# Performance work log

Measured on AMD Instinct MI355X. Metric: run time of the kernel, lower is better.

Reference implementation:

```python
import jax, jax.numpy as jnp
import numpy as np

B, S, E, D, H = 64, 4096, 512, 512, 512
NEG = -1.0e9

def setup_inputs() -> dict:
    key = jax.random.key(0)
    k1, k2, k3, k4, k5, k6 = jax.random.split(key, 6)
    return {
        "enc": jax.random.normal(k1, (B, S, E), dtype=jnp.float32),
        "dec": jax.random.normal(k2, (B, D), dtype=jnp.float32),
        "inp_mask": jax.random.randint(k3, (B, S), 0, 2, dtype=jnp.int32),
        "W_enc": jax.random.normal(k4, (E, H), dtype=jnp.float32),
        "W_dec": jax.random.normal(k5, (D, H), dtype=jnp.float32),
        "W_out": jax.random.normal(k6, (H, 1), dtype=jnp.float32),
    }

def reference(enc, dec, inp_mask, W_enc, W_dec, W_out):
    # Bahdanau additive attention
    encoded = enc @ W_enc                     # [B,S,H]
    decoded = dec @ W_dec                     # [B,H]
    result = jnp.tanh(encoded + decoded[:, None, :])   # [B,S,H]
    logits = jnp.squeeze(result @ W_out, -1)  # [B,S]
    logits = jnp.where(inp_mask == 0, NEG, logits)
    probs = jax.nn.softmax(logits, axis=1)    # [B,S]
    attn = jnp.einsum('bse,bs->be', enc, probs)  # [B,E]
    return (attn, probs)
```

## Files before the change

### kernel.cpp

```cpp
#include <hip/hip_runtime.h>
#include <hip/hip_bf16.h>
#include <cstdint>
#include <cstddef>

#define B_ 64
#define S_ 4096
#define E_ 512
#define H_ 512
#define NEGV (-1.0e9f)

typedef short s8v __attribute__((ext_vector_type(8)));
typedef float f4v __attribute__((ext_vector_type(4)));

__device__ __forceinline__ unsigned short f2bf(float x) {
    unsigned u = __builtin_bit_cast(unsigned, x);
    u = u + 0x7FFFu + ((u >> 16) & 1u);
    return (unsigned short)(u >> 16);
}
__device__ __forceinline__ float bf2f(unsigned short h) {
    unsigned u = ((unsigned)h) << 16;
    return __builtin_bit_cast(float, u);
}

__global__ void prep_w(const float* __restrict__ W_enc,
                       unsigned short* __restrict__ Wt_hi,
                       unsigned short* __restrict__ Wt_lo) {
    int n = blockIdx.x;
    for (int it = 0; it < 2; ++it) {
        int k = threadIdx.x + it * 256;
        float x = W_enc[(size_t)k * H_ + n];
        unsigned short h = f2bf(x);
        float r = x - bf2f(h);
        Wt_hi[(size_t)n * E_ + k] = h;
        Wt_lo[(size_t)n * E_ + k] = f2bf(r);
    }
}

__global__ void dec_proj(const float* __restrict__ dec,
                         const float* __restrict__ W_dec,
                         float* __restrict__ decoded) {
    __shared__ float sd[512];
    int b = blockIdx.x, tid = threadIdx.x;
    sd[tid]       = dec[b * 512 + tid];
    sd[tid + 256] = dec[b * 512 + tid + 256];
    __syncthreads();
    float a0 = 0.f, a1 = 0.f;
#pragma unroll 8
    for (int d = 0; d < 512; ++d) {
        float dv = sd[d];
        a0 += dv * W_dec[(size_t)d * 512 + tid];
        a1 += dv * W_dec[(size_t)d * 512 + tid + 256];
    }
    decoded[b * 512 + tid]       = a0;
    decoded[b * 512 + tid + 256] = a1;
}

__global__ __launch_bounds__(256, 2)
void logits_gemm(const float* __restrict__ enc,
                 const unsigned short* __restrict__ Wt_hi,
                 const unsigned short* __restrict__ Wt_lo,
                 const float* __restrict__ decoded,
                 const float* __restrict__ W_out,
                 float* __restrict__ logits) {
    const int LDA = 40;
    __shared__ __align__(16) unsigned short As_hi[128 * 40];
    __shared__ __align__(16) unsigned short As_lo[128 * 40];
    __shared__ __align__(16) unsigned short Bs_hi[128 * 40];
    __shared__ __align__(16) unsigned short Bs_lo[128 * 40];

    int bx = blockIdx.x;
    int ct = bx & 3, rt = bx >> 2;
    int r0 = rt * 128;
    int b  = r0 >> 12;
    int sb = r0 & 4095;
    int nb0 = ct * 128;

    int tid  = threadIdx.x;
    int lane = tid & 63, wid = tid >> 6;
    int wr = wid >> 1, wc = wid & 1;
    int quad = lane >> 4, cl = lane & 15;

    f4v acc[4][4];
#pragma unroll
    for (int i = 0; i < 4; ++i)
#pragma unroll
        for (int j = 0; j < 4; ++j) acc[i][j] = (f4v)0.f;

    int a_k4 = tid & 7, a_m = tid >> 3;
    int b_k8 = tid & 3, b_n = tid >> 2;

    for (int k0 = 0; k0 < 512; k0 += 32) {
        __syncthreads();
#pragma unroll
        for (int mm = 0; mm < 4; ++mm) {
            int m = a_m + mm * 32;
            float4 v = *(const float4*)(enc + (size_t)(r0 + m) * E_ + k0 + a_k4 * 4);
            unsigned short h0 = f2bf(v.x), h1 = f2bf(v.y), h2 = f2bf(v.z), h3 = f2bf(v.w);
            unsigned short l0 = f2bf(v.x - bf2f(h0)), l1 = f2bf(v.y - bf2f(h1));
            unsigned short l2 = f2bf(v.z - bf2f(h2)), l3 = f2bf(v.w - bf2f(h3));
            uint2 ph, pl;
            ph.x = (unsigned)h0 | ((unsigned)h1 << 16); ph.y = (unsigned)h2 | ((unsigned)h3 << 16);
            pl.x = (unsigned)l0 | ((unsigned)l1 << 16); pl.y = (unsigned)l2 | ((unsigned)l3 << 16);
            *(uint2*)&As_hi[m * LDA + a_k4 * 4] = ph;
            *(uint2*)&As_lo[m * LDA + a_k4 * 4] = pl;
        }
#pragma unroll
        for (int nn = 0; nn < 2; ++nn) {
            int n = b_n + nn * 64;
            *(uint4*)&Bs_hi[n * LDA + b_k8 * 8] =
                *(const uint4*)(Wt_hi + (size_t)(nb0 + n) * E_ + k0 + b_k8 * 8);
            *(uint4*)&Bs_lo[n * LDA + b_k8 * 8] =
                *(const uint4*)(Wt_lo + (size_t)(nb0 + n) * E_ + k0 + b_k8 * 8);
        }
        __syncthreads();

        s8v ah[4], al[4], bh[4], bl[4];
#pragma unroll
        for (int i = 0; i < 4; ++i) {
            int row = wr * 64 + i * 16 + cl;
            ah[i] = *(const s8v*)&As_hi[row * LDA + quad * 8];
            al[i] = *(const s8v*)&As_lo[row * LDA + quad * 8];
        }
#pragma unroll
        for (int j = 0; j < 4; ++j) {
            int col = wc * 64 + j * 16 + cl;
            bh[j] = *(const s8v*)&Bs_hi[col * LDA + quad * 8];
            bl[j] = *(const s8v*)&Bs_lo[col * LDA + quad * 8];
        }
#pragma unroll
        for (int i = 0; i < 4; ++i)
#pragma unroll
            for (int j = 0; j < 4; ++j)
                acc[i][j] = __builtin_amdgcn_mfma_f32_16x16x32_bf16(ah[i], bh[j], acc[i][j], 0, 0, 0);
#pragma unroll
        for (int i = 0; i < 4; ++i)
#pragma unroll
            for (int j = 0; j < 4; ++j)
                acc[i][j] = __builtin_amdgcn_mfma_f32_16x16x32_bf16(ah[i], bl[j], acc[i][j], 0, 0, 0);
#pragma unroll
        for (int i = 0; i < 4; ++i)
#pragma unroll
            for (int j = 0; j < 4; ++j)
                acc[i][j] = __builtin_amdgcn_mfma_f32_16x16x32_bf16(al[i], bh[j], acc[i][j], 0, 0, 0);
    }

    float dcol[4], wcol[4];
#pragma unroll
    for (int j = 0; j < 4; ++j) {
        int h = nb0 + wc * 64 + j * 16 + cl;
        dcol[j] = decoded[b * 512 + h];
        wcol[j] = W_out[h];
    }
#pragma unroll
    for (int i = 0; i < 4; ++i) {
        float rs[4] = {0.f, 0.f, 0.f, 0.f};
#pragma unroll
        for (int j = 0; j < 4; ++j) {
#pragma unroll
            for (int r = 0; r < 4; ++r) {
                float x = acc[i][j][r] + dcol[j];
                float e = __expf(2.0f * x);
                float t = 1.0f - 2.0f / (e + 1.0f);
                rs[r] += t * wcol[j];
            }
        }
#pragma unroll
        for (int r = 0; r < 4; ++r) {
            rs[r] += __shfl_xor(rs[r], 1, 64);
            rs[r] += __shfl_xor(rs[r], 2, 64);
            rs[r] += __shfl_xor(rs[r], 4, 64);
            rs[r] += __shfl_xor(rs[r], 8, 64);
        }
        if (cl == 0) {
            int srow = sb + wr * 64 + i * 16 + quad * 4;
#pragma unroll
            for (int r = 0; r < 4; ++r)
                atomicAdd(&logits[(size_t)b * S_ + srow + r], rs[r]);
        }
    }
}

__global__ void softmax_k(const float* __restrict__ logits,
                          const int* __restrict__ mask,
                          float* __restrict__ probs) {
    __shared__ float red[4];
    int b = blockIdx.x, tid = threadIdx.x;
    int wid = tid >> 6, lane = tid & 63;
    float xs[16];
    float m = -INFINITY;
#pragma unroll
    for (int t = 0; t < 16; ++t) {
        int s = tid + t * 256;
        float x = logits[(size_t)b * S_ + s];
        if (mask[b * S_ + s] == 0) x = NEGV;
        xs[t] = x;
        m = fmaxf(m, x);
    }
#pragma unroll
    for (int off = 32; off >= 1; off >>= 1) m = fmaxf(m, __shfl_xor(m, off, 64));
    if (lane == 0) red[wid] = m;
    __syncthreads();
    m = fmaxf(fmaxf(red[0], red[1]), fmaxf(red[2], red[3]));
    float sum = 0.f;
#pragma unroll
    for (int t = 0; t < 16; ++t) { xs[t] = __expf(xs[t] - m); sum += xs[t]; }
#pragma unroll
    for (int off = 32; off >= 1; off >>= 1) sum += __shfl_xor(sum, off, 64);
    __syncthreads();
    if (lane == 0) red[wid] = sum;
    __syncthreads();
    sum = red[0] + red[1] + red[2] + red[3];
    float inv = 1.0f / sum;
#pragma unroll
    for (int t = 0; t < 16; ++t) probs[(size_t)b * S_ + tid + t * 256] = xs[t] * inv;
}

__global__ void attn_k(const float* __restrict__ enc,
                       const float* __restrict__ probs,
                       float* __restrict__ attn) {
    __shared__ float sp[512];
    int c = blockIdx.x, b = blockIdx.y, tid = threadIdx.x;
    int s0 = c * 512;
    sp[tid]       = probs[(size_t)b * S_ + s0 + tid];
    sp[tid + 256] = probs[(size_t)b * S_ + s0 + tid + 256];
    __syncthreads();
    int e0 = tid * 2;
    float a0 = 0.f, a1 = 0.f;
    for (int ss = 0; ss < 512; ++ss) {
        float p = sp[ss];
        if (p > 1e-8f) {
            const float2 v = *(const float2*)(enc + (size_t)b * S_ * E_ + (size_t)(s0 + ss) * E_ + e0);
            a0 += p * v.x;
            a1 += p * v.y;
        }
    }
    atomicAdd(&attn[b * E_ + e0],     a0);
    atomicAdd(&attn[b * E_ + e0 + 1], a1);
}

extern "C" void kernel_launch(void* const* d_in, const int* in_sizes, int n_in,
                              void* d_out, int out_size, void* d_ws, size_t ws_size,
                              hipStream_t stream) {
    const float* enc   = (const float*)d_in[0];
    const float* dec   = (const float*)d_in[1];
    const int*   mask  = (const int*)d_in[2];
    const float* W_enc = (const float*)d_in[3];
    const float* W_dec = (const float*)d_in[4];
    const float* W_out = (const float*)d_in[5];

    char* ws = (char*)d_ws;
    unsigned short* Wt_hi   = (unsigned short*)(ws);
    unsigned short* Wt_lo   = (unsigned short*)(ws + 524288);
    float*          decoded = (float*)(ws + 1048576);
    float*          logits  = (float*)(ws + 1179648);

    float* attn  = (float*)d_out;
    float* probs = (float*)d_out + B_ * E_;

    hipMemsetAsync(d_out, 0, (size_t)out_size * sizeof(float), stream);
    hipMemsetAsync(logits, 0, (size_t)B_ * S_ * sizeof(float), stream);

    prep_w<<<512, 256, 0, stream>>>(W_enc, Wt_hi, Wt_lo);
    dec_proj<<<B_, 256, 0, stream>>>(dec, W_dec, decoded);
    logits_gemm<<<(B_ * S_ / 128) * 4, 256, 0, stream>>>(enc, Wt_hi, Wt_lo, decoded, W_out, logits);
    softmax_k<<<B_, 256, 0, stream>>>(logits, mask, probs);
    attn_k<<<dim3(8, B_), 256, 0, stream>>>(enc, probs, attn);
}
```

Before: 1.102 ms.

## Fuse softmax with sparse attention pooling, remap GEMM blocks per XCD, split dec_proj

Softmax now also builds a compacted list of nonzero probabilities in shared memory and computes the attention-weighted sum of enc in the same block. This removes the separate attn kernel, its atomics and the output memset. The GEMM block index is remapped so that consecutive row tiles stay on one XCD for L2 reuse, and dec_proj is split across more blocks. The fused pooling runs on only one block per batch, which reduces the parallelism available for streaming enc.

```diff
diff --git a/kernel.cpp b/kernel.cpp
--- a/kernel.cpp
+++ b/kernel.cpp
@@ -12,12 +12,10 @@
 typedef short s8v __attribute__((ext_vector_type(8)));
 typedef float f4v __attribute__((ext_vector_type(4)));
 
-__device__ __forceinline__ unsigned short f2bf(float x) {
-    unsigned u = __builtin_bit_cast(unsigned, x);
-    u = u + 0x7FFFu + ((u >> 16) & 1u);
-    return (unsigned short)(u >> 16);
-}
-__device__ __forceinline__ float bf2f(unsigned short h) {
+__device__ __forceinline__ unsigned short bf_rn(float x) {
+    return __builtin_bit_cast(unsigned short, __float2bfloat16(x));
+}
+__device__ __forceinline__ float bf_up(unsigned short h) {
     unsigned u = ((unsigned)h) << 16;
     return __builtin_bit_cast(float, u);
 }
@@ -29,10 +27,10 @@
     for (int it = 0; it < 2; ++it) {
         int k = threadIdx.x + it * 256;
         float x = W_enc[(size_t)k * H_ + n];
-        unsigned short h = f2bf(x);
-        float r = x - bf2f(h);
+        unsigned short h = bf_rn(x);
+        float r = x - bf_up(h);
         Wt_hi[(size_t)n * E_ + k] = h;
-        Wt_lo[(size_t)n * E_ + k] = f2bf(r);
+        Wt_lo[(size_t)n * E_ + k] = bf_rn(r);
     }
 }
 
@@ -40,19 +38,22 @@
                          const float* __restrict__ W_dec,
                          float* __restrict__ decoded) {
     __shared__ float sd[512];
-    int b = blockIdx.x, tid = threadIdx.x;
+    __shared__ float part[128];
+    int b = blockIdx.y;
+    int h0 = blockIdx.x * 128;
+    int tid = threadIdx.x;
     sd[tid]       = dec[b * 512 + tid];
     sd[tid + 256] = dec[b * 512 + tid + 256];
     __syncthreads();
-    float a0 = 0.f, a1 = 0.f;
+    int h = h0 + (tid & 127);
+    int dh = tid >> 7;
+    float a = 0.f;
 #pragma unroll 8
-    for (int d = 0; d < 512; ++d) {
-        float dv = sd[d];
-        a0 += dv * W_dec[(size_t)d * 512 + tid];
-        a1 += dv * W_dec[(size_t)d * 512 + tid + 256];
-    }
-    decoded[b * 512 + tid]       = a0;
-    decoded[b * 512 + tid + 256] = a1;
+    for (int d = dh * 256; d < dh * 256 + 256; ++d)
+        a += sd[d] * W_dec[(size_t)d * 512 + h];
+    if (dh) part[tid & 127] = a;
+    __syncthreads();
+    if (!dh) decoded[(size_t)b * 512 + h] = a + part[tid];
 }
 
 __global__ __launch_bounds__(256, 2)
@@ -69,7 +70,9 @@
     __shared__ __align__(16) unsigned short Bs_lo[128 * 40];
 
     int bx = blockIdx.x;
-    int ct = bx & 3, rt = bx >> 2;
+    int xcd = bx & 7, idx = bx >> 3;
+    int rt = xcd * 256 + (idx >> 2);
+    int ct = idx & 3;
     int r0 = rt * 128;
     int b  = r0 >> 12;
     int sb = r0 & 4095;
@@ -95,9 +98,9 @@
         for (int mm = 0; mm < 4; ++mm) {
             int m = a_m + mm * 32;
             float4 v = *(const float4*)(enc + (size_t)(r0 + m) * E_ + k0 + a_k4 * 4);
-            unsigned short h0 = f2bf(v.x), h1 = f2bf(v.y), h2 = f2bf(v.z), h3 = f2bf(v.w);
-            unsigned short l0 = f2bf(v.x - bf2f(h0)), l1 = f2bf(v.y - bf2f(h1));
-            unsigned short l2 = f2bf(v.z - bf2f(h2)), l3 = f2bf(v.w - bf2f(h3));
+            unsigned short h0 = bf_rn(v.x), h1 = bf_rn(v.y), h2 = bf_rn(v.z), h3 = bf_rn(v.w);
+            unsigned short l0 = bf_rn(v.x - bf_up(h0)), l1 = bf_rn(v.y - bf_up(h1));
+            unsigned short l2 = bf_rn(v.z - bf_up(h2)), l3 = bf_rn(v.w - bf_up(h3));
             uint2 ph, pl;
             ph.x = (unsigned)h0 | ((unsigned)h1 << 16); ph.y = (unsigned)h2 | ((unsigned)h3 << 16);
             pl.x = (unsigned)l0 | ((unsigned)l1 << 16); pl.y = (unsigned)l2 | ((unsigned)l3 << 16);
@@ -180,12 +183,19 @@
     }
 }
 
-__global__ void softmax_k(const float* __restrict__ logits,
-                          const int* __restrict__ mask,
-                          float* __restrict__ probs) {
+__global__ __launch_bounds__(256)
+void softmax_attn(const float* __restrict__ logits,
+                  const int* __restrict__ mask,
+                  const float* __restrict__ enc,
+                  float* __restrict__ probs,
+                  float* __restrict__ attn) {
     __shared__ float red[4];
+    __shared__ int cnt;
+    __shared__ int   sidx[4096];
+    __shared__ float spv[4096];
     int b = blockIdx.x, tid = threadIdx.x;
     int wid = tid >> 6, lane = tid & 63;
+    if (tid == 0) cnt = 0;
     float xs[16];
     float m = -INFINITY;
 #pragma unroll
@@ -212,30 +222,29 @@
     sum = red[0] + red[1] + red[2] + red[3];
     float inv = 1.0f / sum;
 #pragma unroll
-    for (int t = 0; t < 16; ++t) probs[(size_t)b * S_ + tid + t * 256] = xs[t] * inv;
-}
-
-__global__ void attn_k(const float* __restrict__ enc,
-                       const float* __restrict__ probs,
-                       float* __restrict__ attn) {
-    __shared__ float sp[512];
-    int c = blockIdx.x, b = blockIdx.y, tid = threadIdx.x;
-    int s0 = c * 512;
-    sp[tid]       = probs[(size_t)b * S_ + s0 + tid];
-    sp[tid + 256] = probs[(size_t)b * S_ + s0 + tid + 256];
-    __syncthreads();
+    for (int t = 0; t < 16; ++t) {
+        int s = tid + t * 256;
+        float p = xs[t] * inv;
+        probs[(size_t)b * S_ + s] = p;
+        if (p > 1e-8f) {
+            int k = atomicAdd(&cnt, 1);
+            sidx[k] = s;
+            spv[k]  = p;
+        }
+    }
+    __syncthreads();
+    int n = cnt;
     int e0 = tid * 2;
     float a0 = 0.f, a1 = 0.f;
-    for (int ss = 0; ss < 512; ++ss) {
-        float p = sp[ss];
-        if (p > 1e-8f) {
-            const float2 v = *(const float2*)(enc + (size_t)b * S_ * E_ + (size_t)(s0 + ss) * E_ + e0);
-            a0 += p * v.x;
-            a1 += p * v.y;
-        }
-    }
-    atomicAdd(&attn[b * E_ + e0],     a0);
-    atomicAdd(&attn[b * E_ + e0 + 1], a1);
+    const float* ebase = enc + (size_t)b * S_ * E_ + e0;
+    for (int i = 0; i < n; ++i) {
+        float p = spv[i];
+        const float2 v = *(const float2*)(ebase + (size_t)sidx[i] * E_);
+        a0 += p * v.x;
+        a1 += p * v.y;
+    }
+    attn[b * E_ + e0]     = a0;
+    attn[b * E_ + e0 + 1] = a1;
 }
 
 extern "C" void kernel_launch(void* const* d_in, const int* in_sizes, int n_in,
@@ -257,12 +266,10 @@
     float* attn  = (float*)d_out;
     float* probs = (float*)d_out + B_ * E_;
 
-    hipMemsetAsync(d_out, 0, (size_t)out_size * sizeof(float), stream);
     hipMemsetAsync(logits, 0, (size_t)B_ * S_ * sizeof(float), stream);
 
     prep_w<<<512, 256, 0, stream>>>(W_enc, Wt_hi, Wt_lo);
-    dec_proj<<<B_, 256, 0, stream>>>(dec, W_dec, decoded);
+    dec_proj<<<dim3(4, B_), 256, 0, stream>>>(dec, W_dec, decoded);
     logits_gemm<<<(B_ * S_ / 128) * 4, 256, 0, stream>>>(enc, Wt_hi, Wt_lo, decoded, W_out, logits);
-    softmax_k<<<B_, 256, 0, stream>>>(logits, mask, probs);
-    attn_k<<<dim3(8, B_), 256, 0, stream>>>(enc, probs, attn);
-}
+    softmax_attn<<<B_, 256, 0, stream>>>(logits, mask, enc, probs, attn);
+}
```

Result: faster. 1.017 ms (-7.7%).
